# Kernel optimization log

Hardware: AMD Instinct MI355X
Metric: run time of the kernel (lower is better)

The kernel has to match this reference:

```python
import jax, jax.numpy as jnp
import numpy as np

N_LEVELS = 16
N_FEATS = 2
LOG2_T = 19
BASE_RES = 16.0
FINEST_RES = 512.0
N_POINTS = 1_000_000
HASH_MASK = np.uint32((1 << LOG2_T) - 1)
PRIME1 = np.uint32(2654435761)  # second spatial-hash prime (first is 1)


def setup_inputs() -> dict:
    key = jax.random.key(0)
    k1, k2 = jax.random.split(key)
    x = jax.random.uniform(k1, (N_POINTS, 2), dtype=jnp.float32)
    # nn.init.uniform_(w, -1e-4, 1e-4) per level, stacked: [L, T, F]
    embeddings = (jax.random.uniform(k2, (N_LEVELS, 2 ** LOG2_T, N_FEATS), dtype=jnp.float32) * 2.0 - 1.0) * 1e-4
    return {"x": x, "embeddings": embeddings}


def reference(x, embeddings):
    L = N_LEVELS
    n = x.shape[0]
    # per-level resolutions: floor(base * b**i)
    b = np.exp((np.log(FINEST_RES) - np.log(BASE_RES)) / (L - 1))
    res = np.floor(BASE_RES * b ** np.arange(L)).astype(np.float32)  # [L]
    res_j = jnp.asarray(res)

    pixels = x[None, :, :] * res_j[:, None, None]           # [L, n, 2]
    top_left = jnp.floor(pixels).astype(jnp.int32)          # [L, n, 2]
    offsets = jnp.array([[0, 0], [1, 0], [0, 1], [1, 1]], dtype=jnp.int32)
    box = top_left[:, :, None, :] + offsets[None, None]     # [L, n, 4, 2]
    box = jnp.clip(box, 0, res_j[:, None, None, None].astype(jnp.int32))

    # spatial hash: (c0*1 ^ c1*prime) & mask, with uint32 wraparound like torch int32
    c = box.astype(jnp.uint32)
    addr = ((c[..., 0] * np.uint32(1)) ^ (c[..., 1] * PRIME1)) & HASH_MASK  # [L, n, 4]
    addr = addr.astype(jnp.int32)

    # gather per-level corner features: [L, n, 4, F]
    feats = jax.vmap(lambda table, idx: table[idx])(embeddings, addr)

    # bilinear interpolation
    w = pixels - jnp.floor(pixels)                          # [L, n, 2]
    w0 = w[..., 0:1]
    w1 = w[..., 1:2]
    f0, f1, f2, f3 = feats[:, :, 0], feats[:, :, 1], feats[:, :, 2], feats[:, :, 3]
    f = (f0 * (1 - w0) + f1 * w0) * (1 - w1) + (f2 * (1 - w0) + f3 * w0) * w1  # [L, n, F]

    # concat levels along feature dim -> [n, L*F]
    return jnp.transpose(f, (1, 0, 2)).reshape(n, L * N_FEATS)
```

## Files before the change

kernel.cpp:

```cpp
#include <hip/hip_runtime.h>
#include <hip/hip_fp16.h>
#include <cmath>

#define NLVL 16
#define QUAD_LVLS 13
#define TSIZE (1u << 19)
#define HMASK ((1u << 19) - 1u)
#define PRIME1 2654435761u
#define FSCALE 1024.0f
#define FINV   (1.0f/1024.0f)

typedef float f32x4 __attribute__((ext_vector_type(4)));
typedef unsigned int       u32;
typedef unsigned long long u64;

struct Params {
    float rf[NLVL];
    int   ri[NLVL];
    int   base[NLVL];
    int   stride[NLVL];
};

__device__ __forceinline__ float2 h2f(u32 u) {
    __half2 h; __builtin_memcpy(&h, &u, 4);
    return __half22float2(h);
}

__device__ __forceinline__ u32 packh(float2 v) {
    return (u32)__half_as_ushort(__float2half_rn(v.x * FSCALE))
         | ((u32)__half_as_ushort(__float2half_rn(v.y * FSCALE)) << 16);
}

__global__ __launch_bounds__(256) void build_dense_hyb(
    const float2* __restrict__ emb, u32* __restrict__ dense, Params p)
{
    const int l  = blockIdx.y;
    const int r  = blockIdx.x;
    const int ri = p.ri[l];
    if (r > ri) return;
    const u64* tab = (const u64*)(emb + (size_t)l * TSIZE);
    if (l < QUAD_LVLS) {
        const unsigned hy0 = (unsigned)r * PRIME1;
        const unsigned hy1 = (unsigned)min(r + 1, ri) * PRIME1;
        uint2* drow = (uint2*)(dense + p.base[l]) + (size_t)r * p.stride[l];
        for (int cx = threadIdx.x; cx <= ri; cx += 256) {
            u64 raw0 = __builtin_nontemporal_load(tab + (((unsigned)cx ^ hy0) & HMASK));
            u64 raw1 = __builtin_nontemporal_load(tab + (((unsigned)cx ^ hy1) & HMASK));
            float2 v0, v1;
            __builtin_memcpy(&v0, &raw0, 8);
            __builtin_memcpy(&v1, &raw1, 8);
            uint2 e; e.x = packh(v0); e.y = packh(v1);
            drow[cx] = e;
        }
    } else {
        const unsigned hy = (unsigned)r * PRIME1;
        u32* drow = dense + p.base[l] + (size_t)r * p.stride[l];
        for (int cx = threadIdx.x; cx <= ri; cx += 256) {
            u64 raw = __builtin_nontemporal_load(tab + (((unsigned)cx ^ hy) & HMASK));
            float2 v; __builtin_memcpy(&v, &raw, 8);
            drow[cx] = packh(v);
        }
    }
}

__global__ __launch_bounds__(256) void hash_embed_hyb2(
    const float2* __restrict__ x,
    const u32*    __restrict__ dense,
    float*        __restrict__ out,
    Params p, int n)
{
    __shared__ float lds[8 * 512];
    const int tid = threadIdx.x;
    const int i = blockIdx.x * 256 + tid;
    float2 xy = make_float2(0.f, 0.f);
    if (i < n) {
        u64 raw = __builtin_nontemporal_load((const u64*)(x + i));
        __builtin_memcpy(&xy, &raw, 8);
    }

    const long long total = (long long)n * 32;
    const long long base  = (long long)blockIdx.x * 8192;

    #pragma unroll
    for (int half = 0; half < 2; ++half) {
        uint4 q[8];
        uint2 pa[3], pb[3];
        float w0v[8], w1v[8];
        u32 edgemask = 0;

        #pragma unroll
        for (int j = 0; j < 8; ++j) {
            const int l = half * 8 + j;
            const float rf = p.rf[l];
            const int ri = p.ri[l];
            const float px = xy.x * rf, py = xy.y * rf;
            const float fx = floorf(px), fy = floorf(py);
            w0v[j] = px - fx;
            w1v[j] = py - fy;
            const int tx = (int)fx, ty = (int)fy;
            const int cx0 = min(tx, ri);
            const int cy0 = min(ty, ri);
            edgemask |= (u32)(cx0 == ri) << j;
            if (l < QUAD_LVLS) {
                const uint2* a = (const uint2*)(dense + p.base[l])
                               + cy0 * p.stride[l] + cx0;
                __builtin_memcpy(&q[j], a, 16);
            } else {
                const int m = j - 5;
                const int cy1 = min(ty + 1, ri);
                const u32* tab = dense + p.base[l];
                __builtin_memcpy(&pa[m], tab + cy0 * p.stride[l] + cx0, 8);
                __builtin_memcpy(&pb[m], tab + cy1 * p.stride[l] + cx0, 8);
            }
        }

        if (half == 1) __syncthreads();

        #pragma unroll
        for (int j = 0; j < 8; ++j) {
            const int l = half * 8 + j;
            const float w0 = w0v[j], w1 = w1v[j];
            const float u0 = 1.f - w0, u1 = 1.f - w1;
            const bool ed = (edgemask >> j) & 1u;
            float2 e00, e01, e10, e11;
            if (l < QUAD_LVLS) {
                e00 = h2f(q[j].x);
                e10 = h2f(q[j].y);
                e01 = h2f(ed ? q[j].x : q[j].z);
                e11 = h2f(ed ? q[j].y : q[j].w);
            } else {
                const int m = j - 5;
                e00 = h2f(pa[m].x);
                e01 = h2f(ed ? pa[m].x : pa[m].y);
                e10 = h2f(pb[m].x);
                e11 = h2f(ed ? pb[m].x : pb[m].y);
            }
            const float g0 = ((e00.x*u0 + e01.x*w0)*u1 + (e10.x*u0 + e11.x*w0)*w1) * FINV;
            const float g1 = ((e00.y*u0 + e01.y*w0)*u1 + (e10.y*u0 + e11.y*w0)*w1) * FINV;
            const int idx = j * 512 + ((2 * tid) ^ (j << 1));
            lds[idx]     = g0;
            lds[idx + 1] = g1;
        }
        __syncthreads();

        #pragma unroll
        for (int it = 0; it < 4; ++it) {
            const int f  = (it * 256 + tid) * 4;
            const int p2 = f >> 4;
            const int kk = f & 15;
            const int lh = kk >> 1;
            const long long g = base + (long long)p2 * 32 + half * 16 + kk;
            if (g < total) {
                const int s0 = lh * 512       + ((2 * p2) ^ (lh << 1));
                const int s1 = (lh + 1) * 512 + ((2 * p2) ^ ((lh + 1) << 1));
                f32x4 v;
                v.x = lds[s0]; v.y = lds[s0 + 1];
                v.z = lds[s1]; v.w = lds[s1 + 1];
                __builtin_nontemporal_store(v, (f32x4*)(out + g));
            }
        }
    }
}

__global__ __launch_bounds__(256) void hash_embed_direct(
    const float2* __restrict__ x,
    const float2* __restrict__ emb,
    float* __restrict__ out,
    Params p, int n)
{
    __shared__ float2 lds[NLVL * 256];
    const int tid = threadIdx.x;
    const int i = blockIdx.x * 256 + tid;
    float2 xy = make_float2(0.f, 0.f);
    if (i < n) xy = x[i];

    #pragma unroll
    for (int half = 0; half < 2; ++half) {
        float2 f[32];
        float w0v[8], w1v[8];
        #pragma unroll
        for (int j = 0; j < 8; ++j) {
            const int l = half * 8 + j;
            const float rf = p.rf[l];
            const int ri = p.ri[l];
            const float px = xy.x * rf, py = xy.y * rf;
            const float fx = floorf(px), fy = floorf(py);
            w0v[j] = px - fx;
            w1v[j] = py - fy;
            const int tx = (int)fx, ty = (int)fy;
            const unsigned cx0 = (unsigned)min(tx, ri);
            const unsigned cy0 = (unsigned)min(ty, ri);
            const unsigned cx1 = (unsigned)min(tx + 1, ri);
            const unsigned cy1 = (unsigned)min(ty + 1, ri);
            const unsigned hy0 = cy0 * PRIME1;
            const unsigned hy1 = cy1 * PRIME1;
            const float2* tab = emb + (size_t)l * TSIZE;
            f[j*4+0] = tab[(cx0 ^ hy0) & HMASK];
            f[j*4+1] = tab[(cx1 ^ hy0) & HMASK];
            f[j*4+2] = tab[(cx0 ^ hy1) & HMASK];
            f[j*4+3] = tab[(cx1 ^ hy1) & HMASK];
        }
        #pragma unroll
        for (int j = 0; j < 8; ++j) {
            const int l = half * 8 + j;
            const float w0 = w0v[j], w1 = w1v[j];
            const float u0 = 1.f - w0, u1 = 1.f - w1;
            const float2 f0 = f[j*4+0], f1 = f[j*4+1], f2 = f[j*4+2], f3 = f[j*4+3];
            const float g0 = (f0.x*u0 + f1.x*w0)*u1 + (f2.x*u0 + f3.x*w0)*w1;
            const float g1 = (f0.y*u0 + f1.y*w0)*u1 + (f2.y*u0 + f3.y*w0)*w1;
            lds[l * 256 + tid] = make_float2(g0, g1);
        }
    }
    __syncthreads();

    const float* lf = (const float*)lds;
    const long long total = (long long)n * 32;
    const long long base = (long long)blockIdx.x * 8192;
    #pragma unroll
    for (int it = 0; it < 8; ++it) {
        const int k = (it * 256 + tid) * 4;
        if (base + k < total) {
            const int p2 = k >> 5;
            const int l0 = (k & 31) >> 1;
            float4 v;
            v.x = lf[(l0 * 256 + p2) * 2 + 0];
            v.y = lf[(l0 * 256 + p2) * 2 + 1];
            v.z = lf[((l0 + 1) * 256 + p2) * 2 + 0];
            v.w = lf[((l0 + 1) * 256 + p2) * 2 + 1];
            *(float4*)(out + base + k) = v;
        }
    }
}

extern "C" void kernel_launch(void* const* d_in, const int* in_sizes, int n_in,
                              void* d_out, int out_size, void* d_ws, size_t ws_size,
                              hipStream_t stream) {
    const float2* x = (const float2*)d_in[0];
    const float2* emb = (const float2*)d_in[1];
    float* out = (float*)d_out;
    const int n = in_sizes[0] / 2;

    Params p;
    int off = 0;
    const double b = std::exp((std::log(512.0) - std::log(16.0)) / 15.0);
    for (int l = 0; l < NLVL; ++l) {
        const double r = std::floor(16.0 * std::pow(b, (double)l));
        p.rf[l] = (float)r;
        p.ri[l] = (int)r;
        p.stride[l] = p.ri[l] + 2;
        p.base[l] = off;
        const int cells = (p.ri[l] + 1) * (p.ri[l] + 2);
        off += (l < QUAD_LVLS) ? cells * 2 : cells;
    }
    const size_t need = (size_t)off * sizeof(u32);

    const int grid = (n + 255) / 256;
    if (ws_size >= need) {
        build_dense_hyb<<<dim3(513, 16), 256, 0, stream>>>(emb, (u32*)d_ws, p);
        hash_embed_hyb2<<<grid, 256, 0, stream>>>(x, (const u32*)d_ws, out, p, n);
    } else {
        hash_embed_direct<<<grid, 256, 0, stream>>>(x, emb, out, p, n);
    }
}
```

Measured before the change: 230.2 us.

## Use per-wave LDS transpose regions and overlap second-half gathers with stores

Each wavefront now owns its own LDS slice for transposing interpolated features, so the block-wide __syncthreads barriers are removed and a wave-local lgkmcnt wait is used instead. The gathers for levels 8-15 are issued before the first half's output stores, overlapping memory latency with the stores. Launch bounds now request 8 blocks per CU. This relies on wave-synchronous LDS semantics and raises register pressure because two sets of gathered values are live at once.

New measurement: 319.1 us. +38.6%, slower.

```diff
diff --git a/kernel.cpp b/kernel.cpp
--- a/kernel.cpp
+++ b/kernel.cpp
@@ -63,14 +63,16 @@
     }
 }
 
-__global__ __launch_bounds__(256) void hash_embed_hyb2(
+__global__ __launch_bounds__(256, 8) void hash_embed_hyb3(
     const float2* __restrict__ x,
     const u32*    __restrict__ dense,
     float*        __restrict__ out,
     Params p, int n)
 {
-    __shared__ float lds[8 * 512];
+    __shared__ float lds[16 * 256];
     const int tid = threadIdx.x;
+    const int w   = tid >> 6;
+    const int ln  = tid & 63;
     const int i = blockIdx.x * 256 + tid;
     float2 xy = make_float2(0.f, 0.f);
     if (i < n) {
@@ -78,86 +80,126 @@
         __builtin_memcpy(&xy, &raw, 8);
     }
 
-    const long long total = (long long)n * 32;
-    const long long base  = (long long)blockIdx.x * 8192;
-
-    #pragma unroll
-    for (int half = 0; half < 2; ++half) {
-        uint4 q[8];
-        uint2 pa[3], pb[3];
-        float w0v[8], w1v[8];
-        u32 edgemask = 0;
-
-        #pragma unroll
-        for (int j = 0; j < 8; ++j) {
-            const int l = half * 8 + j;
-            const float rf = p.rf[l];
-            const int ri = p.ri[l];
-            const float px = xy.x * rf, py = xy.y * rf;
-            const float fx = floorf(px), fy = floorf(py);
-            w0v[j] = px - fx;
-            w1v[j] = py - fy;
-            const int tx = (int)fx, ty = (int)fy;
-            const int cx0 = min(tx, ri);
-            const int cy0 = min(ty, ri);
-            edgemask |= (u32)(cx0 == ri) << j;
-            if (l < QUAD_LVLS) {
-                const uint2* a = (const uint2*)(dense + p.base[l])
-                               + cy0 * p.stride[l] + cx0;
-                __builtin_memcpy(&q[j], a, 16);
-            } else {
-                const int m = j - 5;
-                const int cy1 = min(ty + 1, ri);
-                const u32* tab = dense + p.base[l];
-                __builtin_memcpy(&pa[m], tab + cy0 * p.stride[l] + cx0, 8);
-                __builtin_memcpy(&pb[m], tab + cy1 * p.stride[l] + cx0, 8);
-            }
-        }
-
-        if (half == 1) __syncthreads();
-
-        #pragma unroll
-        for (int j = 0; j < 8; ++j) {
-            const int l = half * 8 + j;
-            const float w0 = w0v[j], w1 = w1v[j];
-            const float u0 = 1.f - w0, u1 = 1.f - w1;
-            const bool ed = (edgemask >> j) & 1u;
-            float2 e00, e01, e10, e11;
-            if (l < QUAD_LVLS) {
-                e00 = h2f(q[j].x);
-                e10 = h2f(q[j].y);
-                e01 = h2f(ed ? q[j].x : q[j].z);
-                e11 = h2f(ed ? q[j].y : q[j].w);
-            } else {
-                const int m = j - 5;
-                e00 = h2f(pa[m].x);
-                e01 = h2f(ed ? pa[m].x : pa[m].y);
-                e10 = h2f(pb[m].x);
-                e11 = h2f(ed ? pb[m].x : pb[m].y);
-            }
-            const float g0 = ((e00.x*u0 + e01.x*w0)*u1 + (e10.x*u0 + e11.x*w0)*w1) * FINV;
-            const float g1 = ((e00.y*u0 + e01.y*w0)*u1 + (e10.y*u0 + e11.y*w0)*w1) * FINV;
-            const int idx = j * 512 + ((2 * tid) ^ (j << 1));
-            lds[idx]     = g0;
-            lds[idx + 1] = g1;
-        }
-        __syncthreads();
-
-        #pragma unroll
-        for (int it = 0; it < 4; ++it) {
-            const int f  = (it * 256 + tid) * 4;
-            const int p2 = f >> 4;
-            const int kk = f & 15;
-            const int lh = kk >> 1;
-            const long long g = base + (long long)p2 * 32 + half * 16 + kk;
-            if (g < total) {
-                const int s0 = lh * 512       + ((2 * p2) ^ (lh << 1));
-                const int s1 = (lh + 1) * 512 + ((2 * p2) ^ ((lh + 1) << 1));
-                f32x4 v;
-                v.x = lds[s0]; v.y = lds[s0 + 1];
-                v.z = lds[s1]; v.w = lds[s1 + 1];
-                __builtin_nontemporal_store(v, (f32x4*)(out + g));
-            }
+    const int wbase = w * 1024;
+    const long long ptw = (long long)blockIdx.x * 256 + w * 64;
+
+    uint4 q0[8]; float a_w0[8], a_w1[8]; u32 em0 = 0;
+    #pragma unroll
+    for (int j = 0; j < 8; ++j) {
+        const float rf = p.rf[j];
+        const int ri = p.ri[j];
+        const float px = xy.x * rf, py = xy.y * rf;
+        const float fx = floorf(px), fy = floorf(py);
+        a_w0[j] = px - fx;
+        a_w1[j] = py - fy;
+        const int tx = (int)fx, ty = (int)fy;
+        const int cx0 = min(tx, ri);
+        const int cy0 = min(ty, ri);
+        em0 |= (u32)(cx0 == ri) << j;
+        const uint2* a = (const uint2*)(dense + p.base[j]) + cy0 * p.stride[j] + cx0;
+        __builtin_memcpy(&q0[j], a, 16);
+    }
+    #pragma unroll
+    for (int j = 0; j < 8; ++j) {
+        const float w0 = a_w0[j], w1 = a_w1[j];
+        const float u0 = 1.f - w0, u1 = 1.f - w1;
+        const bool ed = (em0 >> j) & 1u;
+        const float2 e00 = h2f(q0[j].x);
+        const float2 e10 = h2f(q0[j].y);
+        const float2 e01 = h2f(ed ? q0[j].x : q0[j].z);
+        const float2 e11 = h2f(ed ? q0[j].y : q0[j].w);
+        const float g0 = ((e00.x*u0 + e01.x*w0)*u1 + (e10.x*u0 + e11.x*w0)*w1) * FINV;
+        const float g1 = ((e00.y*u0 + e01.y*w0)*u1 + (e10.y*u0 + e11.y*w0)*w1) * FINV;
+        const int idx = wbase + j * 128 + ((2 * ln) ^ (j << 1));
+        lds[idx]     = g0;
+        lds[idx + 1] = g1;
+    }
+
+    uint4 q1[5]; uint2 pa[3], pb[3]; float b_w0[8], b_w1[8]; u32 em1 = 0;
+    #pragma unroll
+    for (int j = 0; j < 8; ++j) {
+        const int l = 8 + j;
+        const float rf = p.rf[l];
+        const int ri = p.ri[l];
+        const float px = xy.x * rf, py = xy.y * rf;
+        const float fx = floorf(px), fy = floorf(py);
+        b_w0[j] = px - fx;
+        b_w1[j] = py - fy;
+        const int tx = (int)fx, ty = (int)fy;
+        const int cx0 = min(tx, ri);
+        const int cy0 = min(ty, ri);
+        em1 |= (u32)(cx0 == ri) << j;
+        if (l < QUAD_LVLS) {
+            const uint2* a = (const uint2*)(dense + p.base[l]) + cy0 * p.stride[l] + cx0;
+            __builtin_memcpy(&q1[j], a, 16);
+        } else {
+            const int m = j - 5;
+            const int cy1 = min(ty + 1, ri);
+            const u32* tab = dense + p.base[l];
+            __builtin_memcpy(&pa[m], tab + cy0 * p.stride[l] + cx0, 8);
+            __builtin_memcpy(&pb[m], tab + cy1 * p.stride[l] + cx0, 8);
+        }
+    }
+
+    #pragma unroll
+    for (int it = 0; it < 4; ++it) {
+        const int k  = (it * 64 + ln) * 4;
+        const int pp = k >> 4;
+        const int kk = k & 15;
+        const int j0 = kk >> 1;
+        const long long pt = ptw + pp;
+        if (pt < n) {
+            const int s0 = wbase + j0 * 128       + ((2 * pp) ^ (j0 << 1));
+            const int s1 = wbase + (j0 + 1) * 128 + ((2 * pp) ^ ((j0 + 1) << 1));
+            f32x4 v;
+            v.x = lds[s0]; v.y = lds[s0 + 1];
+            v.z = lds[s1]; v.w = lds[s1 + 1];
+            __builtin_nontemporal_store(v, (f32x4*)(out + pt * 32 + kk));
+        }
+    }
+
+    asm volatile("s_waitcnt lgkmcnt(0)" ::: "memory");
+
+    #pragma unroll
+    for (int j = 0; j < 8; ++j) {
+        const int l = 8 + j;
+        const float w0 = b_w0[j], w1 = b_w1[j];
+        const float u0 = 1.f - w0, u1 = 1.f - w1;
+        const bool ed = (em1 >> j) & 1u;
+        float2 e00, e01, e10, e11;
+        if (l < QUAD_LVLS) {
+            e00 = h2f(q1[j].x);
+            e10 = h2f(q1[j].y);
+            e01 = h2f(ed ? q1[j].x : q1[j].z);
+            e11 = h2f(ed ? q1[j].y : q1[j].w);
+        } else {
+            const int m = j - 5;
+            e00 = h2f(pa[m].x);
+            e01 = h2f(ed ? pa[m].x : pa[m].y);
+            e10 = h2f(pb[m].x);
+            e11 = h2f(ed ? pb[m].x : pb[m].y);
+        }
+        const float g0 = ((e00.x*u0 + e01.x*w0)*u1 + (e10.x*u0 + e11.x*w0)*w1) * FINV;
+        const float g1 = ((e00.y*u0 + e01.y*w0)*u1 + (e10.y*u0 + e11.y*w0)*w1) * FINV;
+        const int idx = wbase + j * 128 + ((2 * ln) ^ (j << 1));
+        lds[idx]     = g0;
+        lds[idx + 1] = g1;
+    }
+
+    #pragma unroll
+    for (int it = 0; it < 4; ++it) {
+        const int k  = (it * 64 + ln) * 4;
+        const int pp = k >> 4;
+        const int kk = k & 15;
+        const int j0 = kk >> 1;
+        const long long pt = ptw + pp;
+        if (pt < n) {
+            const int s0 = wbase + j0 * 128       + ((2 * pp) ^ (j0 << 1));
+            const int s1 = wbase + (j0 + 1) * 128 + ((2 * pp) ^ ((j0 + 1) << 1));
+            f32x4 v;
+            v.x = lds[s0]; v.y = lds[s0 + 1];
+            v.z = lds[s1]; v.w = lds[s1 + 1];
+            __builtin_nontemporal_store(v, (f32x4*)(out + pt * 32 + 16 + kk));
         }
     }
 }
@@ -257,7 +299,7 @@
     const int grid = (n + 255) / 256;
     if (ws_size >= need) {
         build_dense_hyb<<<dim3(513, 16), 256, 0, stream>>>(emb, (u32*)d_ws, p);
-        hash_embed_hyb2<<<grid, 256, 0, stream>>>(x, (const u32*)d_ws, out, p, n);
+        hash_embed_hyb3<<<grid, 256, 0, stream>>>(x, (const u32*)d_ws, out, p, n);
     } else {
         hash_embed_direct<<<grid, 256, 0, stream>>>(x, emb, out, p, n);
     }
```
